# Performance work log

Measured on AMD Instinct MI355X. Metric: run time of the kernel, lower is better.

Reference implementation:

```python
import jax, jax.numpy as jnp
import numpy as np

D_MODEL = 2048
EXPAND = 2
D_INNER = EXPAND * D_MODEL          # 4096 == d_ssm
D_STATE = 128
NGROUPS = 1
HEADDIM = 64
NHEADS = D_INNER // HEADDIM          # 64
D_CONV = 4
CHUNK = 128
D_XBC = D_INNER + 2 * NGROUPS * D_STATE   # 4352
D_IN_PROJ = 2 * D_INNER + 2 * NGROUPS * D_STATE + NHEADS  # 8512
EPS = 1e-5


def setup_inputs() -> dict:
    key = jax.random.key(0)
    ks = jax.random.split(key, 9)
    u = jax.random.normal(ks[0], (2, 2048, D_MODEL), dtype=jnp.float32)
    W_in = jax.random.normal(ks[1], (D_IN_PROJ, D_MODEL), dtype=jnp.float32) / np.sqrt(D_MODEL)
    conv_w = jax.random.normal(ks[2], (D_XBC, D_CONV), dtype=jnp.float32) / np.sqrt(D_CONV)
    conv_b = jax.random.normal(ks[3], (D_XBC,), dtype=jnp.float32) * 0.1
    dt_bias = jnp.log(jnp.expm1(jax.random.uniform(ks[4], (NHEADS,), minval=0.001, maxval=0.1)))
    A_log = jnp.log(jax.random.uniform(ks[5], (NHEADS,), minval=1.0, maxval=16.0))
    D = jnp.ones((NHEADS,), dtype=jnp.float32)
    norm_weight = jnp.ones((D_INNER,), dtype=jnp.float32)
    W_out = jax.random.normal(ks[8], (D_MODEL, D_INNER), dtype=jnp.float32) / np.sqrt(D_INNER)
    return {"u": u, "W_in": W_in, "conv_w": conv_w, "conv_b": conv_b,
            "dt_bias": dt_bias, "A_log": A_log, "D": D,
            "norm_weight": norm_weight, "W_out": W_out}


def _causal_conv1d(xBC, conv_w, conv_b):
    # xBC: [b, l, d]; depthwise causal conv of width D_CONV, then SiLU
    x = jnp.transpose(xBC, (0, 2, 1))                      # [b, d, l]
    x = jnp.pad(x, ((0, 0), (0, 0), (D_CONV - 1, 0)))
    y = jax.lax.conv_general_dilated(
        x, conv_w[:, None, :], window_strides=(1,), padding='VALID',
        feature_group_count=D_XBC, dimension_numbers=('NCH', 'OIH', 'NCH'))
    y = y + conv_b[None, :, None]
    return jnp.transpose(jax.nn.silu(y), (0, 2, 1))        # [b, l, d]


def _ssd(x, dt, A, B, C, D):
    # x: [b,l,h,p]; dt: [b,l,h] (post-softplus); A: [h]; B,C: [b,l,g,n]; D: [h]
    b, L, h, p = x.shape
    n = B.shape[-1]
    c = L // CHUNK
    hpg = h // NGROUPS
    Bh = jnp.repeat(B, hpg, axis=2)                        # [b,l,h,n]
    Ch = jnp.repeat(C, hpg, axis=2)
    xr = x.reshape(b, c, CHUNK, h, p)
    dtr = dt.reshape(b, c, CHUNK, h)
    Br = Bh.reshape(b, c, CHUNK, h, n)
    Cr = Ch.reshape(b, c, CHUNK, h, n)
    xdt = xr * dtr[..., None]                              # [b,c,l,h,p]
    dA = jnp.transpose((dt * A[None, None, :]).reshape(b, c, CHUNK, h), (0, 3, 1, 2))  # [b,h,c,l]
    A_cs = jnp.cumsum(dA, axis=-1)                         # [b,h,c,l]
    # intra-chunk decay matrix L[i,j] = exp(sum_{j+1..i} dA), lower-triangular
    diff = A_cs[..., :, None] - A_cs[..., None, :]         # [b,h,c,l,s]
    mask = jnp.tril(jnp.ones((CHUNK, CHUNK), dtype=bool))
    Lmat = jnp.where(mask, jnp.exp(jnp.where(mask, diff, 0.0)), 0.0)
    Y_diag = jnp.einsum('bclhn,bcshn,bhcls,bcshp->bclhp', Cr, Br, Lmat, xdt)
    decay_states = jnp.exp(A_cs[..., -1:] - A_cs)          # [b,h,c,l]
    states = jnp.einsum('bclhn,bhcl,bclhp->bchpn', Br, decay_states, xdt)
    chunk_decay = jnp.exp(A_cs[..., -1])                   # [b,h,c]
    # inter-chunk recurrence over c chunks
    def step(carry, inp):
        s, d = inp                                         # s:[b,h,p,n], d:[b,h]
        return carry * d[..., None, None] + s, carry
    init = jnp.zeros((b, h, p, n), dtype=x.dtype)
    _, prev = jax.lax.scan(step, init,
                           (jnp.transpose(states, (1, 0, 2, 3, 4)),
                            jnp.transpose(chunk_decay, (2, 0, 1))))
    prev_states = jnp.transpose(prev, (1, 0, 2, 3, 4))     # [b,c,h,p,n]
    Y_off = jnp.einsum('bclhn,bchpn,bhcl->bclhp', Cr, prev_states, jnp.exp(A_cs))
    Y = (Y_diag + Y_off).reshape(b, L, h, p) + x * D[None, None, :, None]
    return Y


def reference(u, W_in, conv_w, conv_b, dt_bias, A_log, D, norm_weight, W_out):
    b, L, _ = u.shape
    zxbcdt = jnp.einsum('bld,ed->ble', u, W_in)            # [b,l,8512]
    z = zxbcdt[..., :D_INNER]
    xBC = zxbcdt[..., D_INNER:D_INNER + D_XBC]
    dt = zxbcdt[..., D_INNER + D_XBC:]                     # [b,l,h]
    xBC = _causal_conv1d(xBC, conv_w, conv_b)
    x = xBC[..., :D_INNER]
    B = xBC[..., D_INNER:D_INNER + NGROUPS * D_STATE].reshape(b, L, NGROUPS, D_STATE)
    C = xBC[..., D_INNER + NGROUPS * D_STATE:].reshape(b, L, NGROUPS, D_STATE)
    dt = jax.nn.softplus(dt + dt_bias[None, None, :])
    A = -jnp.exp(A_log)
    y = _ssd(x.reshape(b, L, NHEADS, HEADDIM), dt, A, B, C, D)
    y = y.reshape(b, L, D_INNER)
    # gated RMSNorm (norm_before_gate=False): norm(y * silu(z))
    yg = y * jax.nn.silu(z)
    y = yg * jax.lax.rsqrt(jnp.mean(yg * yg, axis=-1, keepdims=True) + EPS) * norm_weight
    return jnp.einsum('bld,ed->ble', y, W_out)
```

## Files before the change

kernel.cpp:

```cpp
#include <hip/hip_runtime.h>
#include <cstdint>
#include <cstddef>

#define SEQ     2048
#define NBATCH  2
#define BL      (NBATCH*SEQ)
#define DMODEL  2048
#define DINNER  4096
#define DSTATE  128
#define HEADDIM 64
#define NHEADS  64
#define DXBC    4352
#define DPROJ   8512
#define NPAD    8576
#define NCHUNK  16
#define CHUNKL  128

typedef __bf16 bf16x8_t __attribute__((ext_vector_type(8)));
typedef float f32x4_t __attribute__((ext_vector_type(4)));
typedef unsigned short u16x8_t __attribute__((ext_vector_type(8)));
typedef unsigned short u16x4_t __attribute__((ext_vector_type(4)));
typedef __attribute__((address_space(1))) unsigned int as1_u32;
typedef __attribute__((address_space(3))) unsigned int as3_u32;

__device__ __forceinline__ unsigned short f2bf(float f) {
  unsigned u = __builtin_bit_cast(unsigned, f);
  u += 0x7FFFu + ((u >> 16) & 1u);
  return (unsigned short)(u >> 16);
}
__device__ __forceinline__ float bf2f(unsigned short h) {
  unsigned u = ((unsigned)h) << 16;
  return __builtin_bit_cast(float, u);
}
__device__ __forceinline__ void gload16(const void* g, void* l) {
  __builtin_amdgcn_global_load_lds((const as1_u32*)g, (as3_u32*)l, 16, 0, 0);
}
__device__ __forceinline__ f32x4_t mfma16(u16x8_t a, u16x8_t b, f32x4_t c) {
  return __builtin_amdgcn_mfma_f32_16x16x32_bf16(
      __builtin_bit_cast(bf16x8_t, a), __builtin_bit_cast(bf16x8_t, b), c, 0, 0, 0);
}
__device__ __forceinline__ float siluf(float x) { return x / (1.f + __expf(-x)); }

__global__ __launch_bounds__(256) void cvt_kernel(const float* __restrict__ src,
                                                  unsigned short* __restrict__ dst, int n) {
  int idx = (blockIdx.x * 256 + threadIdx.x) * 4;
  if (idx >= n) return;
  float4 v = *(const float4*)&src[idx];
  u16x4_t o; o[0] = f2bf(v.x); o[1] = f2bf(v.y); o[2] = f2bf(v.z); o[3] = f2bf(v.w);
  *(u16x4_t*)&dst[idx] = o;
}

__global__ __launch_bounds__(256) void cvt_win_kernel(const float* __restrict__ W,
                                                      unsigned short* __restrict__ dst) {
  int idx = (blockIdx.x * 256 + threadIdx.x) * 4;
  if (idx >= NPAD * DMODEL) return;
  int e = idx / DMODEL;
  u16x4_t o;
  if (e < DPROJ) {
    float4 v = *(const float4*)&W[idx];
    o[0] = f2bf(v.x); o[1] = f2bf(v.y); o[2] = f2bf(v.z); o[3] = f2bf(v.w);
  } else {
    o[0] = 0; o[1] = 0; o[2] = 0; o[3] = 0;
  }
  *(u16x4_t*)&dst[idx] = o;
}

template <bool BF16OUT>
__global__ __launch_bounds__(256) void gemm_bt_kernel(const unsigned short* __restrict__ A,
                                                      const unsigned short* __restrict__ B,
                                                      void* __restrict__ Cp,
                                                      int M, int N, int K, int gx) {
  __shared__ unsigned short As[128 * 64];
  __shared__ unsigned short Bs[128 * 64];
  const int nwg = gridDim.x;
  const int q = nwg >> 3;
  const int l = blockIdx.x;
  const int newid = (l & 7) * q + (l >> 3);
  const int band = newid / (gx * 4);
  const int idx  = newid % (gx * 4);
  const int bn = idx >> 2;
  const int bm = band * 4 + (idx & 3);
  const int n0 = bn * 128;
  const int m0 = bm * 128;
  const int t = threadIdx.x, lane = t & 63, w = t >> 6;
  const int wr = w >> 1, wc = w & 1;
  const int srow = t >> 3;
  const int scol = (t & 7) * 8;
  f32x4_t acc[4][4];
#pragma unroll
  for (int i = 0; i < 4; ++i)
#pragma unroll
    for (int j = 0; j < 4; ++j) acc[i][j] = (f32x4_t){0.f, 0.f, 0.f, 0.f};

  const int nk = K >> 6;
  for (int kt = 0; kt < nk; ++kt) {
    const int k0 = kt << 6;
#pragma unroll
    for (int s = 0; s < 4; ++s) {
      int r = s * 32 + srow;
      gload16(&A[(size_t)(m0 + r) * K + k0 + scol], &As[r * 64 + scol]);
      gload16(&B[(size_t)(n0 + r) * K + k0 + scol], &Bs[r * 64 + scol]);
    }
    __syncthreads();
#pragma unroll
    for (int ks = 0; ks < 2; ++ks) {
      const int kk = ks * 32 + (lane >> 4) * 8;
      u16x8_t af[4], bfr[4];
#pragma unroll
      for (int i = 0; i < 4; ++i) {
        af[i]  = *(const u16x8_t*)&As[(wr * 64 + i * 16 + (lane & 15)) * 64 + kk];
        bfr[i] = *(const u16x8_t*)&Bs[(wc * 64 + i * 16 + (lane & 15)) * 64 + kk];
      }
#pragma unroll
      for (int i = 0; i < 4; ++i)
#pragma unroll
        for (int j = 0; j < 4; ++j) acc[i][j] = mfma16(af[i], bfr[j], acc[i][j]);
    }
    __syncthreads();
  }
#pragma unroll
  for (int i = 0; i < 4; ++i) {
    const int mbase = m0 + wr * 64 + i * 16 + (lane >> 4) * 4;
#pragma unroll
    for (int j = 0; j < 4; ++j) {
      const int n = n0 + wc * 64 + j * 16 + (lane & 15);
#pragma unroll
      for (int r = 0; r < 4; ++r) {
        if (BF16OUT) ((unsigned short*)Cp)[(size_t)(mbase + r) * N + n] = f2bf(acc[i][j][r]);
        else         ((float*)Cp)[(size_t)(mbase + r) * N + n] = acc[i][j][r];
      }
    }
  }
}

__global__ __launch_bounds__(256) void conv_kernel(const unsigned short* __restrict__ zx,
                                                   const float* __restrict__ conv_w,
                                                   const float* __restrict__ conv_b,
                                                   unsigned short* __restrict__ xc) {
  long long idx = (long long)blockIdx.x * 256 + threadIdx.x;
  if (idx >= (long long)BL * DXBC) return;
  int e = (int)(idx % DXBC);
  int bl = (int)(idx / DXBC);
  int l = bl % SEQ, b = bl / SEQ;
  float acc = conv_b[e];
#pragma unroll
  for (int wi = 0; wi < 4; ++wi) {
    int ll = l - 3 + wi;
    if (ll >= 0) acc += bf2f(zx[((size_t)b * SEQ + ll) * NPAD + DINNER + e]) * conv_w[e * 4 + wi];
  }
  xc[(size_t)bl * DXBC + e] = f2bf(siluf(acc));
}

__global__ __launch_bounds__(128) void dt_kernel(const unsigned short* __restrict__ zx,
                                                 const float* __restrict__ dt_bias,
                                                 const float* __restrict__ A_log,
                                                 float* __restrict__ dt_soft,
                                                 float* __restrict__ Acs,
                                                 float* __restrict__ cdecay) {
  int blk = blockIdx.x;
  int c = blk & 15, h = (blk >> 4) & 63, b = blk >> 10;
  int i = threadIdx.x;
  int l = c * CHUNKL + i;
  float raw = bf2f(zx[((size_t)b * SEQ + l) * NPAD + (DINNER + DXBC) + h]) + dt_bias[h];
  float dt = (raw > 20.f) ? raw : log1pf(__expf(raw));
  dt_soft[((size_t)b * 64 + h) * SEQ + l] = dt;
  float A = -__expf(A_log[h]);
  __shared__ float sbuf[128];
  sbuf[i] = dt * A;
  __syncthreads();
  for (int ofs = 1; ofs < 128; ofs <<= 1) {
    float v = (i >= ofs) ? sbuf[i - ofs] : 0.f;
    __syncthreads();
    sbuf[i] += v;
    __syncthreads();
  }
  float cs = sbuf[i];
  Acs[(((size_t)b * 64 + h) * 16 + c) * 128 + i] = cs;
  if (i == 127) cdecay[((size_t)b * 64 + h) * 16 + c] = __expf(cs);
}

__global__ __launch_bounds__(256) void xdt_kernel(const unsigned short* __restrict__ xc,
                                                  const float* __restrict__ dt_soft,
                                                  unsigned short* __restrict__ xdtT) {
  int blk = blockIdx.x;
  int lt = blk & 15, h = (blk >> 4) & 63, b = blk >> 10;
  __shared__ unsigned short tile[128][66];
  __shared__ float dts[128];
  int t = threadIdx.x;
  const unsigned short* xg = xc + ((size_t)b * SEQ + lt * 128) * DXBC + h * 64;
#pragma unroll
  for (int k = 0; k < 32; ++k) {
    int idx = t + k * 256;
    int row = idx >> 6, col = idx & 63;
    tile[row][col] = xg[(size_t)row * DXBC + col];
  }
  if (t < 128) dts[t] = dt_soft[((size_t)b * 64 + h) * SEQ + lt * 128 + t];
  __syncthreads();
  unsigned short* xo = xdtT + (((size_t)b * 64 + h) * 64) * SEQ + lt * 128;
#pragma unroll
  for (int k = 0; k < 32; ++k) {
    int idx = t + k * 256;
    int p = idx >> 7, j = idx & 127;
    xo[(size_t)p * SEQ + j] = f2bf(bf2f(tile[j][p]) * dts[j]);
  }
}

__global__ __launch_bounds__(256) void btr_kernel(const unsigned short* __restrict__ xc,
                                                  unsigned short* __restrict__ BT) {
  int blk = blockIdx.x;
  int lt = blk & 15, b = blk >> 4;
  __shared__ unsigned short tile[128][129];
  int t = threadIdx.x;
  const unsigned short* src = xc + ((size_t)b * SEQ + lt * 128) * DXBC + DINNER;
#pragma unroll
  for (int k = 0; k < 64; ++k) {
    int idx = t + k * 256;
    int j = idx >> 7, n = idx & 127;
    tile[j][n] = src[(size_t)j * DXBC + n];
  }
  __syncthreads();
  unsigned short* dst = BT + (size_t)b * 128 * SEQ + lt * 128;
#pragma unroll
  for (int k = 0; k < 64; ++k) {
    int idx = t + k * 256;
    int n = idx >> 7, j = idx & 127;
    dst[(size_t)n * SEQ + j] = tile[j][n];
  }
}

__global__ __launch_bounds__(256) void ssd_states_kernel(const unsigned short* __restrict__ BT,
                                                         const unsigned short* __restrict__ xdtT,
                                                         const float* __restrict__ Acs,
                                                         float* __restrict__ states) {
  int blk = blockIdx.x;
  int h = blk & 63, c = (blk >> 6) & 15, b = blk >> 10;
  __shared__ unsigned short BTs[128 * 128];
  __shared__ unsigned short xs[64 * 128];
  __shared__ float dec[128];
  int t = threadIdx.x, lane = t & 63, w = t >> 6, wr = w >> 1, wc = w & 1;
  int srow = t >> 4, scol = (t & 15) * 8;
  const unsigned short* BTb = BT + (size_t)b * 128 * SEQ + c * 128;
#pragma unroll
  for (int s = 0; s < 8; ++s) {
    int r = s * 16 + srow;
    gload16(&BTb[(size_t)r * SEQ + scol], &BTs[r * 128 + scol]);
  }
  const unsigned short* xb = xdtT + (((size_t)b * 64 + h) * 64) * SEQ + c * 128;
#pragma unroll
  for (int s = 0; s < 4; ++s) {
    int r = s * 16 + srow;
    gload16(&xb[(size_t)r * SEQ + scol], &xs[r * 128 + scol]);
  }
  const float* acsr = Acs + (((size_t)b * 64 + h) * 16 + c) * 128;
  float alast = acsr[127];
  if (t < 128) dec[t] = __expf(alast - acsr[t]);
  __syncthreads();

  f32x4_t acc[2][4];
#pragma unroll
  for (int i = 0; i < 2; ++i)
#pragma unroll
    for (int j = 0; j < 4; ++j) acc[i][j] = (f32x4_t){0.f, 0.f, 0.f, 0.f};
#pragma unroll
  for (int ks = 0; ks < 4; ++ks) {
    const int kk = ks * 32 + (lane >> 4) * 8;
    float d8[8];
#pragma unroll
    for (int e = 0; e < 8; ++e) d8[e] = dec[kk + e];
    u16x8_t af[2], bfr[4];
#pragma unroll
    for (int i = 0; i < 2; ++i) {
      u16x8_t raw = *(const u16x8_t*)&xs[(wr * 32 + i * 16 + (lane & 15)) * 128 + kk];
      u16x8_t sc;
#pragma unroll
      for (int e = 0; e < 8; ++e) sc[e] = f2bf(bf2f(raw[e]) * d8[e]);
      af[i] = sc;
    }
#pragma unroll
    for (int j = 0; j < 4; ++j)
      bfr[j] = *(const u16x8_t*)&BTs[(wc * 64 + j * 16 + (lane & 15)) * 128 + kk];
#pragma unroll
    for (int i = 0; i < 2; ++i)
#pragma unroll
      for (int j = 0; j < 4; ++j) acc[i][j] = mfma16(af[i], bfr[j], acc[i][j]);
  }
  float* so = states + ((((size_t)b * 16 + c) * 64 + h) * 64) * 128;
#pragma unroll
  for (int i = 0; i < 2; ++i) {
    int pbase = wr * 32 + i * 16 + (lane >> 4) * 4;
#pragma unroll
    for (int j = 0; j < 4; ++j) {
      int n = wc * 64 + j * 16 + (lane & 15);
#pragma unroll
      for (int r = 0; r < 4; ++r) so[(size_t)(pbase + r) * 128 + n] = acc[i][j][r];
    }
  }
}

__global__ __launch_bounds__(256) void ssd_scan_kernel(const float* __restrict__ states,
                                                       const float* __restrict__ cdecay,
                                                       unsigned short* __restrict__ prevb) {
  int blk = blockIdx.x;
  int s = blk & 7, h = (blk >> 3) & 63, b = blk >> 9;
  int t = threadIdx.x;
  float carry[4] = {0.f, 0.f, 0.f, 0.f};
  const float* cd = cdecay + ((size_t)b * 64 + h) * 16;
  const size_t hoff = ((size_t)b * 16) * 64 + h;
  for (int c = 0; c < 16; ++c) {
    const float* sp = states + (((size_t)(b * 16 + c) * 64 + h) * 64) * 128;
    unsigned short* pp = prevb + (((size_t)(b * 16 + c) * 64 + h) * 64) * 128;
    float d = cd[c];
#pragma unroll
    for (int k = 0; k < 4; ++k) {
      int e = s * 1024 + k * 256 + t;
      pp[e] = f2bf(carry[k]);
      carry[k] = carry[k] * d + sp[e];
    }
  }
  (void)hoff;
}

__global__ __launch_bounds__(256) void ssd_y_kernel(const unsigned short* __restrict__ xc,
                                                    const unsigned short* __restrict__ xdtT,
                                                    const unsigned short* __restrict__ prevb,
                                                    const float* __restrict__ Acs,
                                                    const float* __restrict__ Dp,
                                                    unsigned short* __restrict__ Y) {
  int blk = blockIdx.x;
  int h = blk & 63, c = (blk >> 6) & 15, b = blk >> 10;
  __shared__ unsigned short Bs[128 * 128];
  __shared__ unsigned short Cs[128 * 128];
  __shared__ unsigned short xs[64 * 128];
  __shared__ unsigned short ps[64 * 128];
  __shared__ float acs_s[128];
  int t = threadIdx.x, lane = t & 63, w = t >> 6, wr = w >> 1, wc = w & 1;
  int srow = t >> 4, scol = (t & 15) * 8;
  const unsigned short* Bg = xc + ((size_t)b * SEQ + c * 128) * DXBC + DINNER;
  const unsigned short* Cg = Bg + DSTATE;
#pragma unroll
  for (int s = 0; s < 8; ++s) {
    int r = s * 16 + srow;
    gload16(&Bg[(size_t)r * DXBC + scol], &Bs[r * 128 + scol]);
    gload16(&Cg[(size_t)r * DXBC + scol], &Cs[r * 128 + scol]);
  }
  const unsigned short* xg = xdtT + (((size_t)b * 64 + h) * 64) * SEQ + c * 128;
#pragma unroll
  for (int s = 0; s < 4; ++s) {
    int r = s * 16 + srow;
    gload16(&xg[(size_t)r * SEQ + scol], &xs[r * 128 + scol]);
  }
  const unsigned short* pg = prevb + ((((size_t)b * 16 + c) * 64 + h) * 64) * 128;
#pragma unroll
  for (int s = 0; s < 4; ++s) {
    int r = s * 16 + srow;
    gload16(&pg[r * 128 + scol], &ps[r * 128 + scol]);
  }
  const float* acsr = Acs + (((size_t)b * 64 + h) * 16 + c) * 128;
  if (t < 128) acs_s[t] = acsr[t];
  __syncthreads();

  f32x4_t cbt[4][4];
#pragma unroll
  for (int i = 0; i < 4; ++i)
#pragma unroll
    for (int j = 0; j < 4; ++j) cbt[i][j] = (f32x4_t){0.f, 0.f, 0.f, 0.f};
#pragma unroll
  for (int ks = 0; ks < 4; ++ks) {
    const int kk = ks * 32 + (lane >> 4) * 8;
    u16x8_t af[4], bfr[4];
#pragma unroll
    for (int i = 0; i < 4; ++i) {
      af[i]  = *(const u16x8_t*)&Bs[(wr * 64 + i * 16 + (lane & 15)) * 128 + kk];
      bfr[i] = *(const u16x8_t*)&Cs[(wc * 64 + i * 16 + (lane & 15)) * 128 + kk];
    }
#pragma unroll
    for (int i = 0; i < 4; ++i)
#pragma unroll
      for (int j = 0; j < 4; ++j) cbt[i][j] = mfma16(af[i], bfr[j], cbt[i][j]);
  }
  __syncthreads();
#pragma unroll
  for (int fi = 0; fi < 4; ++fi) {
#pragma unroll
    for (int fj = 0; fj < 4; ++fj) {
      int i = wc * 64 + fj * 16 + (lane & 15);
      int jb = wr * 64 + fi * 16 + (lane >> 4) * 4;
      float ai = acs_s[i];
      u16x4_t m4;
#pragma unroll
      for (int r = 0; r < 4; ++r) {
        int j = jb + r;
        float v = (i >= j) ? cbt[fi][fj][r] * __expf(ai - acs_s[j]) : 0.f;
        m4[r] = f2bf(v);
      }
      *(u16x4_t*)&Bs[i * 128 + jb] = m4;
    }
  }
  __syncthreads();

  f32x4_t accY[4][2], accO[4][2];
#pragma unroll
  for (int i = 0; i < 4; ++i)
#pragma unroll
    for (int j = 0; j < 2; ++j) {
      accY[i][j] = (f32x4_t){0.f, 0.f, 0.f, 0.f};
      accO[i][j] = (f32x4_t){0.f, 0.f, 0.f, 0.f};
    }
#pragma unroll
  for (int ks = 0; ks < 4; ++ks) {
    const int kk = ks * 32 + (lane >> 4) * 8;
    u16x8_t af[4], bfr[2], cf[4], pf[2];
#pragma unroll
    for (int i = 0; i < 4; ++i) {
      af[i] = *(const u16x8_t*)&Bs[(wr * 64 + i * 16 + (lane & 15)) * 128 + kk];
      cf[i] = *(const u16x8_t*)&Cs[(wr * 64 + i * 16 + (lane & 15)) * 128 + kk];
    }
#pragma unroll
    for (int j = 0; j < 2; ++j) {
      bfr[j] = *(const u16x8_t*)&xs[(wc * 32 + j * 16 + (lane & 15)) * 128 + kk];
      pf[j]  = *(const u16x8_t*)&ps[(wc * 32 + j * 16 + (lane & 15)) * 128 + kk];
    }
#pragma unroll
    for (int i = 0; i < 4; ++i)
#pragma unroll
      for (int j = 0; j < 2; ++j) {
        accY[i][j] = mfma16(af[i], bfr[j], accY[i][j]);
        accO[i][j] = mfma16(cf[i], pf[j], accO[i][j]);
      }
  }
  float Dh = Dp[h];
  unsigned short* Yo = Y + ((size_t)b * SEQ + c * 128) * DINNER + h * 64;
  const unsigned short* xo = xc + ((size_t)b * SEQ + c * 128) * DXBC + h * 64;
#pragma unroll
  for (int fi = 0; fi < 4; ++fi) {
    int ibase = wr * 64 + fi * 16 + (lane >> 4) * 4;
#pragma unroll
    for (int r = 0; r < 4; ++r) {
      int i = ibase + r;
      float esc = __expf(acs_s[i]);
#pragma unroll
      for (int fj = 0; fj < 2; ++fj) {
        int p = wc * 32 + fj * 16 + (lane & 15);
        float v = accY[fi][fj][r] + accO[fi][fj][r] * esc + bf2f(xo[(size_t)i * DXBC + p]) * Dh;
        Yo[(size_t)i * DINNER + p] = f2bf(v);
      }
    }
  }
}

__global__ __launch_bounds__(256) void norm_kernel(const unsigned short* __restrict__ Y,
                                                   const unsigned short* __restrict__ zx,
                                                   const float* __restrict__ nw,
                                                   unsigned short* __restrict__ yn) {
  int bl = blockIdx.x;
  const unsigned short* yr = Y + (size_t)bl * DINNER;
  const unsigned short* zr = zx + (size_t)bl * NPAD;
  int t = threadIdx.x;
  float vals[16];
  float ss = 0.f;
#pragma unroll
  for (int k = 0; k < 16; ++k) {
    int d = t + k * 256;
    float g = bf2f(yr[d]) * siluf(bf2f(zr[d]));
    vals[k] = g;
    ss += g * g;
  }
#pragma unroll
  for (int o = 32; o > 0; o >>= 1) ss += __shfl_down(ss, o, 64);
  __shared__ float red[4];
  if ((t & 63) == 0) red[t >> 6] = ss;
  __syncthreads();
  float tot = red[0] + red[1] + red[2] + red[3];
  float rs = rsqrtf(tot * (1.f / (float)DINNER) + 1e-5f);
#pragma unroll
  for (int k = 0; k < 16; ++k) {
    int d = t + k * 256;
    yn[(size_t)bl * DINNER + d] = f2bf(vals[k] * rs * nw[d]);
  }
}

extern "C" void kernel_launch(void* const* d_in, const int* in_sizes, int n_in,
                              void* d_out, int out_size, void* d_ws, size_t ws_size,
                              hipStream_t stream) {
  const float* u       = (const float*)d_in[0];
  const float* W_in    = (const float*)d_in[1];
  const float* conv_w  = (const float*)d_in[2];
  const float* conv_b  = (const float*)d_in[3];
  const float* dt_bias = (const float*)d_in[4];
  const float* A_log   = (const float*)d_in[5];
  const float* Dv      = (const float*)d_in[6];
  const float* norm_w  = (const float*)d_in[7];
  const float* W_out   = (const float*)d_in[8];
  float* out = (float*)d_out;
  (void)in_sizes; (void)n_in; (void)out_size;

  const size_t SZ_UBF    = (size_t)BL * DMODEL * 2;
  const size_t SZ_WIN    = (size_t)NPAD * DMODEL * 2;
  const size_t SZ_XDTT   = (size_t)NBATCH * NHEADS * HEADDIM * SEQ * 2;
  const size_t SZ_ZX     = (size_t)BL * NPAD * 2;
  const size_t SZ_XC     = (size_t)BL * DXBC * 2;
  const size_t SZ_BT     = (size_t)NBATCH * DSTATE * SEQ * 2;
  const size_t SZ_DTS    = (size_t)NBATCH * NHEADS * SEQ * 4;
  const size_t SZ_ACS    = (size_t)NBATCH * NHEADS * NCHUNK * 128 * 4;
  const size_t SZ_CDEC   = (size_t)NBATCH * NHEADS * NCHUNK * 4;
  const size_t SZ_STATES = (size_t)NBATCH * NCHUNK * NHEADS * HEADDIM * DSTATE * 4;
  const size_t SZ_PREV   = (size_t)NBATCH * NCHUNK * NHEADS * HEADDIM * DSTATE * 2;
  const size_t REGION_A  = SZ_UBF + SZ_WIN;

  char* ws = (char*)d_ws;
  size_t off = 0;
  auto alloc = [&](size_t bytes) { char* p = ws + off; off += (bytes + 255) & ~(size_t)255; return p; };

  char* regionA = alloc(REGION_A);
  unsigned short* zx     = (unsigned short*)alloc(SZ_ZX);
  unsigned short* xc     = (unsigned short*)alloc(SZ_XC);
  unsigned short* BT     = (unsigned short*)alloc(SZ_BT);
  float* dt_soft         = (float*)alloc(SZ_DTS);
  float* Acs             = (float*)alloc(SZ_ACS);
  float* cdecay          = (float*)alloc(SZ_CDEC);
  char* statesYb         = alloc(SZ_STATES);
  char* prevYn           = alloc(SZ_PREV);
  if (off > ws_size) return;

  unsigned short* u_bf    = (unsigned short*)regionA;
  unsigned short* win_bf  = (unsigned short*)(regionA + SZ_UBF);
  unsigned short* xdtT    = (unsigned short*)regionA;
  unsigned short* wout_bf = (unsigned short*)(regionA + SZ_XDTT);
  float* states           = (float*)statesYb;
  unsigned short* Yb      = (unsigned short*)statesYb;
  unsigned short* prevb   = (unsigned short*)prevYn;
  unsigned short* yn      = (unsigned short*)prevYn;

  cvt_kernel<<<dim3((BL * DMODEL / 4 + 255) / 256), dim3(256), 0, stream>>>(u, u_bf, BL * DMODEL);
  cvt_win_kernel<<<dim3(NPAD * DMODEL / 4 / 256), dim3(256), 0, stream>>>(W_in, win_bf);

  gemm_bt_kernel<true><<<dim3((NPAD / 128) * (BL / 128)), dim3(256), 0, stream>>>(
      u_bf, win_bf, zx, BL, NPAD, DMODEL, NPAD / 128);

  cvt_kernel<<<dim3((DMODEL * DINNER / 4 + 255) / 256), dim3(256), 0, stream>>>(W_out, wout_bf, DMODEL * DINNER);

  conv_kernel<<<dim3((int)(((size_t)BL * DXBC + 255) / 256)), dim3(256), 0, stream>>>(zx, conv_w, conv_b, xc);

  dt_kernel<<<dim3(NBATCH * NHEADS * NCHUNK), dim3(128), 0, stream>>>(zx, dt_bias, A_log, dt_soft, Acs, cdecay);

  xdt_kernel<<<dim3(NBATCH * NHEADS * NCHUNK), dim3(256), 0, stream>>>(xc, dt_soft, xdtT);
  btr_kernel<<<dim3(NBATCH * (SEQ / 128)), dim3(256), 0, stream>>>(xc, BT);

  ssd_states_kernel<<<dim3(NBATCH * NCHUNK * NHEADS), dim3(256), 0, stream>>>(BT, xdtT, Acs, states);
  ssd_scan_kernel<<<dim3(NBATCH * NHEADS * 8), dim3(256), 0, stream>>>(states, cdecay, prevb);
  ssd_y_kernel<<<dim3(NBATCH * NCHUNK * NHEADS), dim3(256), 0, stream>>>(xc, xdtT, prevb, Acs, Dv, Yb);

  norm_kernel<<<dim3(BL), dim3(256), 0, stream>>>(Yb, zx, norm_w, yn);

  gemm_bt_kernel<false><<<dim3((DMODEL / 128) * (BL / 128)), dim3(256), 0, stream>>>(
      yn, wout_bf, out, BL, DMODEL, DINNER, DMODEL / 128);
}
```

Baseline: 628.6 us.

## Replace GEMMs with 256x256-tile kernel using a 4-stage swizzled LDS pipeline

Swaps the 128x128 bf16 MFMA GEMM for a 512-thread 256x256-tile kernel. It keeps a 4-deep ring of K=32 slices in LDS with an XOR-swizzled layout and uses explicit vmcnt waits so global loads overlap the MFMA work. It also interleaves staging with the matrix ops and raises wave priority around the MFMA bursts. The projection width is padded to a multiple of 256 to match the new tile. The risks are lower occupancy and fewer workgroups: the output projection launches only 128 blocks, which may leave many CUs idle.

Measured after the change: 579.7 us. 1.08x faster.

```diff
diff --git a/kernel.cpp b/kernel.cpp
--- a/kernel.cpp
+++ b/kernel.cpp
@@ -12,7 +12,7 @@
 #define NHEADS  64
 #define DXBC    4352
 #define DPROJ   8512
-#define NPAD    8576
+#define NPAD    8704
 #define NCHUNK  16
 #define CHUNKL  128
 
@@ -66,68 +66,106 @@
 }
 
 template <bool BF16OUT>
-__global__ __launch_bounds__(256) void gemm_bt_kernel(const unsigned short* __restrict__ A,
-                                                      const unsigned short* __restrict__ B,
-                                                      void* __restrict__ Cp,
-                                                      int M, int N, int K, int gx) {
-  __shared__ unsigned short As[128 * 64];
-  __shared__ unsigned short Bs[128 * 64];
+__global__ __launch_bounds__(512, 2) void gemm256_kernel(const unsigned short* __restrict__ A,
+                                                         const unsigned short* __restrict__ B,
+                                                         void* __restrict__ Cp,
+                                                         int M, int N, int K, int gx) {
+  __shared__ unsigned short lds[65536];
   const int nwg = gridDim.x;
-  const int q = nwg >> 3;
-  const int l = blockIdx.x;
-  const int newid = (l & 7) * q + (l >> 3);
+  const int q8 = nwg >> 3;
+  const int lid = blockIdx.x;
+  const int newid = (lid & 7) * q8 + (lid >> 3);
   const int band = newid / (gx * 4);
   const int idx  = newid % (gx * 4);
-  const int bn = idx >> 2;
-  const int bm = band * 4 + (idx & 3);
-  const int n0 = bn * 128;
-  const int m0 = bm * 128;
+  const int n0 = (idx >> 2) * 256;
+  const int m0 = (band * 4 + (idx & 3)) * 256;
+
   const int t = threadIdx.x, lane = t & 63, w = t >> 6;
-  const int wr = w >> 1, wc = w & 1;
-  const int srow = t >> 3;
-  const int scol = (t & 7) * 8;
-  f32x4_t acc[4][4];
-#pragma unroll
-  for (int i = 0; i < 4; ++i)
+  const int wm = w >> 2, wn = w & 3;
+  const int NK = K >> 5;
+
+  f32x4_t acc[8][4];
+#pragma unroll
+  for (int i = 0; i < 8; ++i)
 #pragma unroll
     for (int j = 0; j < 4; ++j) acc[i][j] = (f32x4_t){0.f, 0.f, 0.f, 0.f};
 
-  const int nk = K >> 6;
-  for (int kt = 0; kt < nk; ++kt) {
-    const int k0 = kt << 6;
-#pragma unroll
-    for (int s = 0; s < 4; ++s) {
-      int r = s * 32 + srow;
-      gload16(&A[(size_t)(m0 + r) * K + k0 + scol], &As[r * 64 + scol]);
-      gload16(&B[(size_t)(n0 + r) * K + k0 + scol], &Bs[r * 64 + scol]);
-    }
-    __syncthreads();
-#pragma unroll
-    for (int ks = 0; ks < 2; ++ks) {
-      const int kk = ks * 32 + (lane >> 4) * 8;
-      u16x8_t af[4], bfr[4];
-#pragma unroll
-      for (int i = 0; i < 4; ++i) {
-        af[i]  = *(const u16x8_t*)&As[(wr * 64 + i * 16 + (lane & 15)) * 64 + kk];
-        bfr[i] = *(const u16x8_t*)&Bs[(wc * 64 + i * 16 + (lane & 15)) * 64 + kk];
-      }
-#pragma unroll
-      for (int i = 0; i < 4; ++i)
-#pragma unroll
-        for (int j = 0; j < 4; ++j) acc[i][j] = mfma16(af[i], bfr[j], acc[i][j]);
-    }
-    __syncthreads();
-  }
-#pragma unroll
-  for (int i = 0; i < 4; ++i) {
-    const int mbase = m0 + wr * 64 + i * 16 + (lane >> 4) * 4;
-#pragma unroll
-    for (int j = 0; j < 4; ++j) {
-      const int n = n0 + wc * 64 + j * 16 + (lane & 15);
+  auto stage_unit = [&](int u) {
+    if (u >= 2 * NK) return;
+    const int Tt = u >> 1;
+    const unsigned short* G = (u & 1) ? B : A;
+    const int g0 = (u & 1) ? n0 : m0;
+    const int k0 = Tt << 5;
+    char* base = (char*)lds + ((Tt & 3) * 32768 + (u & 1) * 16384);
+#pragma unroll
+    for (int i = 0; i < 2; ++i) {
+      int o = i * 8192 + t * 16;
+      int row = o >> 6;
+      int cb = (o & 63) ^ (((row >> 1) & 3) << 4);
+      gload16(&G[(size_t)(g0 + row) * K + k0 + (cb >> 1)], base + o);
+    }
+  };
+
+#pragma unroll
+  for (int u = 0; u < 6; ++u) stage_unit(u);
+
+  for (int T = 0; T < NK; ++T) {
+    const int Tq = (T & 3) * 32768;
+    if (T <= NK - 3)      asm volatile("s_waitcnt vmcnt(8)" ::: "memory");
+    else if (T == NK - 2) asm volatile("s_waitcnt vmcnt(4)" ::: "memory");
+    else                  asm volatile("s_waitcnt vmcnt(0)" ::: "memory");
+    __builtin_amdgcn_s_barrier();
+    asm volatile("" ::: "memory");
+    __builtin_amdgcn_sched_barrier(0);
+
+    const int kslot = (lane >> 4) * 16;
+    u16x8_t af[8], bfr[4];
+#pragma unroll
+    for (int mr = 0; mr < 8; ++mr) {
+      int row = wm * 128 + mr * 16 + (lane & 15);
+      int byte = Tq + row * 64 + (kslot ^ (((row >> 1) & 3) << 4));
+      af[mr] = *(const u16x8_t*)((const char*)lds + byte);
+    }
+#pragma unroll
+    for (int nr = 0; nr < 2; ++nr) {
+      int row = wn * 64 + nr * 16 + (lane & 15);
+      int byte = Tq + 16384 + row * 64 + (kslot ^ (((row >> 1) & 3) << 4));
+      bfr[nr] = *(const u16x8_t*)((const char*)lds + byte);
+    }
+    stage_unit(2 * T + 6);
+    __builtin_amdgcn_s_setprio(1);
+#pragma unroll
+    for (int mr = 0; mr < 8; ++mr) {
+      acc[mr][0] = mfma16(af[mr], bfr[0], acc[mr][0]);
+      acc[mr][1] = mfma16(af[mr], bfr[1], acc[mr][1]);
+    }
+    __builtin_amdgcn_s_setprio(0);
+#pragma unroll
+    for (int nr = 2; nr < 4; ++nr) {
+      int row = wn * 64 + nr * 16 + (lane & 15);
+      int byte = Tq + 16384 + row * 64 + (kslot ^ (((row >> 1) & 3) << 4));
+      bfr[nr] = *(const u16x8_t*)((const char*)lds + byte);
+    }
+    stage_unit(2 * T + 7);
+    __builtin_amdgcn_s_setprio(1);
+#pragma unroll
+    for (int mr = 0; mr < 8; ++mr) {
+      acc[mr][2] = mfma16(af[mr], bfr[2], acc[mr][2]);
+      acc[mr][3] = mfma16(af[mr], bfr[3], acc[mr][3]);
+    }
+    __builtin_amdgcn_s_setprio(0);
+  }
+
+#pragma unroll
+  for (int mr = 0; mr < 8; ++mr) {
+    const int mbase = m0 + wm * 128 + mr * 16 + (lane >> 4) * 4;
+#pragma unroll
+    for (int nr = 0; nr < 4; ++nr) {
+      const int n = n0 + wn * 64 + nr * 16 + (lane & 15);
 #pragma unroll
       for (int r = 0; r < 4; ++r) {
-        if (BF16OUT) ((unsigned short*)Cp)[(size_t)(mbase + r) * N + n] = f2bf(acc[i][j][r]);
-        else         ((float*)Cp)[(size_t)(mbase + r) * N + n] = acc[i][j][r];
+        if (BF16OUT) ((unsigned short*)Cp)[(size_t)(mbase + r) * N + n] = f2bf(acc[mr][nr][r]);
+        else         ((float*)Cp)[(size_t)(mbase + r) * N + n] = acc[mr][nr][r];
       }
     }
   }
@@ -305,7 +343,6 @@
   int t = threadIdx.x;
   float carry[4] = {0.f, 0.f, 0.f, 0.f};
   const float* cd = cdecay + ((size_t)b * 64 + h) * 16;
-  const size_t hoff = ((size_t)b * 16) * 64 + h;
   for (int c = 0; c < 16; ++c) {
     const float* sp = states + (((size_t)(b * 16 + c) * 64 + h) * 64) * 128;
     unsigned short* pp = prevb + (((size_t)(b * 16 + c) * 64 + h) * 64) * 128;
@@ -317,7 +354,6 @@
       carry[k] = carry[k] * d + sp[e];
     }
   }
-  (void)hoff;
 }
 
 __global__ __launch_bounds__(256) void ssd_y_kernel(const unsigned short* __restrict__ xc,
@@ -534,8 +570,8 @@
   cvt_kernel<<<dim3((BL * DMODEL / 4 + 255) / 256), dim3(256), 0, stream>>>(u, u_bf, BL * DMODEL);
   cvt_win_kernel<<<dim3(NPAD * DMODEL / 4 / 256), dim3(256), 0, stream>>>(W_in, win_bf);
 
-  gemm_bt_kernel<true><<<dim3((NPAD / 128) * (BL / 128)), dim3(256), 0, stream>>>(
-      u_bf, win_bf, zx, BL, NPAD, DMODEL, NPAD / 128);
+  gemm256_kernel<true><<<dim3((NPAD / 256) * (BL / 256)), dim3(512), 0, stream>>>(
+      u_bf, win_bf, zx, BL, NPAD, DMODEL, NPAD / 256);
 
   cvt_kernel<<<dim3((DMODEL * DINNER / 4 + 255) / 256), dim3(256), 0, stream>>>(W_out, wout_bf, DMODEL * DINNER);
 
@@ -552,6 +588,6 @@
 
   norm_kernel<<<dim3(BL), dim3(256), 0, stream>>>(Yb, zx, norm_w, yn);
 
-  gemm_bt_kernel<false><<<dim3((DMODEL / 128) * (BL / 128)), dim3(256), 0, stream>>>(
-      yn, wout_bf, out, BL, DMODEL, DINNER, DMODEL / 128);
-}
+  gemm256_kernel<false><<<dim3((DMODEL / 256) * (BL / 256)), dim3(512), 0, stream>>>(
+      yn, wout_bf, out, BL, DMODEL, DINNER, DMODEL / 256);
+}
```
